# Kernel optimization log

Hardware: AMD Instinct MI355X
Metric: run time of the kernel (lower is better)

Reference implementation:

```python
import jax, jax.numpy as jnp
import numpy as np

# ---- static configuration (matches init_kwargs) ----
B = 256              # graph pairs -> 2B graphs total (query/corpus interleaved)
N_PER_GRAPH = 24     # nodes per graph
N_MAX = 32           # max node set size (transport plan side)
E_PER_GRAPH = 200    # edges per graph
E_MAX = 256          # max_edge_set_size
D_EDGE = 256         # edge_feature_dim
D_SINK = 256         # sinkhorn_feature_dim
TEMPERATURE = 0.1
NUM_SINKHORN_ITERS = 20
NOISE_FACTOR = 0.0   # deterministic sinkhorn
CONSISTENCY_WEIGHT = 1.0


def setup_inputs() -> dict:
    rng = np.random.RandomState(0)
    num_graphs = 2 * B
    node_offset = np.arange(num_graphs) * N_PER_GRAPH
    graph_idx = np.repeat(np.arange(num_graphs), N_PER_GRAPH)
    # edges are grouped by graph (standard batched-graph layout)
    from_local = rng.randint(0, N_PER_GRAPH, size=(num_graphs, E_PER_GRAPH))
    to_local = rng.randint(0, N_PER_GRAPH, size=(num_graphs, E_PER_GRAPH))
    from_idx = (from_local + node_offset[:, None]).reshape(-1)
    to_idx = (to_local + node_offset[:, None]).reshape(-1)
    total_edges = num_graphs * E_PER_GRAPH

    key = jax.random.key(0)
    k = jax.random.split(key, 4)
    return {
        "edge_features_enc": jax.random.normal(k[0], (total_edges, D_EDGE), jnp.float32),
        "node_transport_plan": jax.random.uniform(k[1], (B, N_MAX, N_MAX), jnp.float32),
        "W1": jax.random.normal(k[2], (D_EDGE, D_SINK), jnp.float32) / np.sqrt(D_EDGE).astype(np.float32),
        "b1": jnp.zeros((D_SINK,), jnp.float32),
        "W2": jax.random.normal(k[3], (D_SINK, D_SINK), jnp.float32) / np.sqrt(D_SINK).astype(np.float32),
        "b2": jnp.zeros((D_SINK,), jnp.float32),
        "from_idx": jnp.asarray(from_idx, jnp.int32),
        "to_idx": jnp.asarray(to_idx, jnp.int32),
        "graph_idx": jnp.asarray(graph_idx, jnp.int32),
        "query_sizes": jnp.full((B,), N_PER_GRAPH, jnp.int32),
        "corpus_sizes": jnp.full((B,), N_PER_GRAPH, jnp.int32),
    }


def reference(edge_features_enc, node_transport_plan, W1, b1, W2, b2,
              from_idx, to_idx, graph_idx, query_sizes, corpus_sizes):
    num_graphs = 2 * B
    total_edges = from_idx.shape[0]

    # --- get_paired_edge_counts / split_and_stack ---
    g_edge = graph_idx[from_idx]                                   # graph id per edge
    edge_counts = jax.ops.segment_sum(jnp.ones_like(g_edge), g_edge, num_segments=num_graphs)
    edge_offset = jnp.cumsum(edge_counts) - edge_counts            # exclusive prefix
    rank = jnp.arange(total_edges, dtype=jnp.int32) - edge_offset[g_edge]

    stacked = jnp.zeros((num_graphs, E_MAX, D_EDGE), edge_features_enc.dtype)
    stacked = stacked.at[g_edge, rank].set(edge_features_enc)      # [2B, E_MAX, D]
    q_feat, c_feat = stacked[0::2], stacked[1::2]

    # --- sinkhorn_feature_layers (Linear-ReLU-Linear) + size mask ---
    def mlp(x):
        return jax.nn.relu(x @ W1 + b1) @ W2 + b2
    q_feat, c_feat = mlp(q_feat), mlp(c_feat)
    pos = jnp.arange(E_MAX)
    q_feat = q_feat * (pos[None, :] < query_sizes[:, None]).astype(q_feat.dtype)[..., None]
    c_feat = c_feat * (pos[None, :] < corpus_sizes[:, None]).astype(c_feat.dtype)[..., None]

    # --- kronecker_product_on_nodes: local endpoint ids, pad slots -> zero row N_MAX ---
    node_counts = jax.ops.segment_sum(jnp.ones_like(graph_idx), graph_idx, num_segments=num_graphs)
    node_offset = jnp.cumsum(node_counts) - node_counts
    pad = jnp.full((num_graphs, E_MAX), N_MAX, jnp.int32)
    f_loc = pad.at[g_edge, rank].set(from_idx - node_offset[g_edge])
    t_loc = pad.at[g_edge, rank].set(to_idx - node_offset[g_edge])
    fq, fc = f_loc[0::2], f_loc[1::2]
    tq, tc = t_loc[0::2], t_loc[1::2]

    T = jnp.pad(node_transport_plan, ((0, 0), (0, 1), (0, 1)))     # zero row/col for pads
    b = jnp.arange(B)[:, None, None]
    straight = T[b, fq[:, :, None], fc[:, None, :]] * T[b, tq[:, :, None], tc[:, None, :]]
    cross = T[b, fq[:, :, None], tc[:, None, :]] * T[b, tq[:, :, None], fc[:, None, :]]

    # --- sinkhorn_iters (log domain, noise_factor=0) ---
    log_alpha = (straight + cross) / TEMPERATURE                   # [B, E_MAX, E_MAX]
    def step(la, _):
        la = la - jax.nn.logsumexp(la, axis=2, keepdims=True)
        la = la - jax.nn.logsumexp(la, axis=1, keepdims=True)
        return la, None
    log_alpha, _ = jax.lax.scan(step, log_alpha, None, length=NUM_SINKHORN_ITERS)
    plan = jnp.exp(log_alpha)

    # --- feature_alignment_score: -sum(relu(q - P c)) per pair ---
    score = -jax.nn.relu(q_feat - plan @ c_feat).sum(axis=(1, 2))
    return CONSISTENCY_WEIGHT * score
```

## Files before the change

### kernel.cpp

```cpp
#include <hip/hip_runtime.h>

typedef unsigned short ushort_t;
typedef unsigned int uint_t;

typedef float f32x4_t __attribute__((ext_vector_type(4)));
typedef short s16x8_t __attribute__((ext_vector_type(8)));

#define NB   256
#define NG   512
#define NPG  24
#define NMAXI 32
#define EPG  200
#define DD   256
#define L2E_OVER_T 14.426950408889634f

__device__ __forceinline__ ushort_t f2bf(float f) {
    uint_t u = __float_as_uint(f);
    u += 0x7FFFu + ((u >> 16) & 1u);
    return (ushort_t)(u >> 16);
}
__device__ __forceinline__ float bfhi(uint_t u) { return __uint_as_float(u & 0xFFFF0000u); }
__device__ __forceinline__ float bflo(uint_t u) { return __uint_as_float(u << 16); }

__device__ __forceinline__ float frcp(float x) {
#if __has_builtin(__builtin_amdgcn_rcpf)
    return __builtin_amdgcn_rcpf(x);
#else
    return 1.0f / x;
#endif
}

__global__ __launch_bounds__(256) void prep_w(const float* __restrict__ W1,
                                              const float* __restrict__ W2,
                                              ushort_t* __restrict__ W1T,
                                              ushort_t* __restrict__ W2T)
{
    __shared__ float tile[2][4 * 256];
    const int t = threadIdx.x;
    const int k0 = blockIdx.x * 4;
    #pragma unroll
    for (int i = t; i < 4 * 256; i += 256) {
        tile[0][i] = W1[k0 * 256 + i];
        tile[1][i] = W2[k0 * 256 + i];
    }
    __syncthreads();
    const int n = t;
    #pragma unroll
    for (int m = 0; m < 2; ++m) {
        uint_t p0 = (uint_t)f2bf(tile[m][0 * 256 + n]) | ((uint_t)f2bf(tile[m][1 * 256 + n]) << 16);
        uint_t p1 = (uint_t)f2bf(tile[m][2 * 256 + n]) | ((uint_t)f2bf(tile[m][3 * 256 + n]) << 16);
        ushort_t* dst = (m ? W2T : W1T) + n * 256 + k0;
        uint2 pk; pk.x = p0; pk.y = p1;
        *(uint2*)dst = pk;
    }
}

__global__ __launch_bounds__(256) void mlp_kernel(
    const float* __restrict__ X, const ushort_t* __restrict__ W1T,
    const ushort_t* __restrict__ W2T, const float* __restrict__ b1,
    const float* __restrict__ b2, float* __restrict__ Y)
{
    __shared__ ushort_t sA[64 * 272];
    const int t = threadIdx.x;
    const int blk = blockIdx.x;
    const int lane = t & 63;
    const int w = t >> 6;
    const int quad = lane >> 4;
    const int mrow = lane & 15;

    {
        int r = t >> 2;
        int ch = (t & 3) * 64;
        int rho = blk * 64 + r;
        int g = rho / NPG;
        int e = rho - g * NPG;
        const float* src = X + ((size_t)(g * EPG + e)) * DD + ch;
        ushort_t* dst = &sA[r * 272 + ch];
        #pragma unroll
        for (int i = 0; i < 8; ++i) {
            float4 v0 = *(const float4*)(src + i * 8);
            float4 v1 = *(const float4*)(src + i * 8 + 4);
            uint4 pk;
            pk.x = (uint_t)f2bf(v0.x) | ((uint_t)f2bf(v0.y) << 16);
            pk.y = (uint_t)f2bf(v0.z) | ((uint_t)f2bf(v0.w) << 16);
            pk.z = (uint_t)f2bf(v1.x) | ((uint_t)f2bf(v1.y) << 16);
            pk.w = (uint_t)f2bf(v1.z) | ((uint_t)f2bf(v1.w) << 16);
            *(uint4*)(dst + i * 8) = pk;
        }
    }
    __syncthreads();

    f32x4_t acc[16];
    #pragma unroll
    for (int i = 0; i < 16; ++i) acc[i] = (f32x4_t){0.f, 0.f, 0.f, 0.f};

    #pragma unroll
    for (int k0 = 0; k0 < 256; k0 += 32) {
        s16x8_t a[4], bb[4];
        #pragma unroll
        for (int mt = 0; mt < 4; ++mt)
            a[mt] = *(const s16x8_t*)&sA[(mt * 16 + mrow) * 272 + k0 + quad * 8];
        #pragma unroll
        for (int nt = 0; nt < 4; ++nt)
            bb[nt] = *(const s16x8_t*)(W1T + (size_t)(64 * w + nt * 16 + mrow) * 256 + k0 + quad * 8);
        #pragma unroll
        for (int mt = 0; mt < 4; ++mt) {
            #pragma unroll
            for (int nt = 0; nt < 4; ++nt)
                acc[mt * 4 + nt] = __builtin_amdgcn_mfma_f32_16x16x32_bf16(
                    a[mt], bb[nt], acc[mt * 4 + nt], 0, 0, 0);
        }
    }
    __syncthreads();

    #pragma unroll
    for (int nt = 0; nt < 4; ++nt) {
        int col = 64 * w + nt * 16 + mrow;
        float bias = b1[col];
        #pragma unroll
        for (int mt = 0; mt < 4; ++mt) {
            f32x4_t v = acc[mt * 4 + nt];
            #pragma unroll
            for (int reg = 0; reg < 4; ++reg) {
                int row = mt * 16 + quad * 4 + reg;
                sA[row * 272 + col] = f2bf(fmaxf(v[reg] + bias, 0.f));
            }
        }
    }
    __syncthreads();

    #pragma unroll
    for (int i = 0; i < 16; ++i) acc[i] = (f32x4_t){0.f, 0.f, 0.f, 0.f};

    #pragma unroll
    for (int k0 = 0; k0 < 256; k0 += 32) {
        s16x8_t a[4], bb[4];
        #pragma unroll
        for (int mt = 0; mt < 4; ++mt)
            a[mt] = *(const s16x8_t*)&sA[(mt * 16 + mrow) * 272 + k0 + quad * 8];
        #pragma unroll
        for (int nt = 0; nt < 4; ++nt)
            bb[nt] = *(const s16x8_t*)(W2T + (size_t)(64 * w + nt * 16 + mrow) * 256 + k0 + quad * 8);
        #pragma unroll
        for (int mt = 0; mt < 4; ++mt) {
            #pragma unroll
            for (int nt = 0; nt < 4; ++nt)
                acc[mt * 4 + nt] = __builtin_amdgcn_mfma_f32_16x16x32_bf16(
                    a[mt], bb[nt], acc[mt * 4 + nt], 0, 0, 0);
        }
    }

    #pragma unroll
    for (int nt = 0; nt < 4; ++nt) {
        int col = 64 * w + nt * 16 + mrow;
        float bias = b2[col];
        #pragma unroll
        for (int mt = 0; mt < 4; ++mt) {
            f32x4_t v = acc[mt * 4 + nt];
            #pragma unroll
            for (int reg = 0; reg < 4; ++reg) {
                int row = blk * 64 + mt * 16 + quad * 4 + reg;
                Y[(size_t)row * 256 + col] = v[reg] + bias;
            }
        }
    }
}

__global__ __launch_bounds__(1024) void sink_kernel(
    const float* __restrict__ Tplan, const int* __restrict__ from_idx,
    const int* __restrict__ to_idx, const int* __restrict__ qsz,
    const int* __restrict__ csz, const float* __restrict__ qcf,
    float* __restrict__ out)
{
    const int b = blockIdx.x;
    const int t = threadIdx.x;
    const int R = t >> 4;
    const int C = t & 15;
    const int w = t >> 6;

    __shared__ __align__(16) char ovl[56320];
    __shared__ float ru_s[260];
    __shared__ float rv_p[320];
    __shared__ float wsum[16];

    float* Tl = (float*)ovl;
    int* fq = (int*)(ovl + 4368);
    int* tq = (int*)(ovl + 5392);
    int* fc = (int*)(ovl + 6416);
    int* tc = (int*)(ovl + 7440);
    float* Vp = (float*)ovl;
    ushort_t* planb = (ushort_t*)ovl;
    ushort_t* cftb  = (ushort_t*)(ovl + 20480);

    for (int i = t; i < 33 * 33; i += 1024) Tl[i] = 0.f;
    if (t < 320) rv_p[t] = 1.0f;
    if (t < 256) {
        int gq = 2 * b, gc = 2 * b + 1;
        int a = NMAXI, bb = NMAXI, c = NMAXI, d = NMAXI;
        if (t < EPG) {
            a  = from_idx[gq * EPG + t] - gq * NPG;
            bb = to_idx  [gq * EPG + t] - gq * NPG;
            c  = from_idx[gc * EPG + t] - gc * NPG;
            d  = to_idx  [gc * EPG + t] - gc * NPG;
        }
        fq[t] = a; tq[t] = bb; fc[t] = c; tc[t] = d;
    }
    __syncthreads();
    {
        int i = t >> 5, j = t & 31;
        Tl[i * 33 + j] = Tplan[((size_t)b << 10) + t];
    }
    __syncthreads();

    uint_t Kp[4][8];
    {
        const float* T1a = &Tl[fq[4 * R + 0] * 33];
        const float* T2a = &Tl[tq[4 * R + 0] * 33];
        const float* T1b = &Tl[fq[4 * R + 1] * 33];
        const float* T2b = &Tl[tq[4 * R + 1] * 33];
        const float* T1c = &Tl[fq[4 * R + 2] * 33];
        const float* T2c = &Tl[tq[4 * R + 2] * 33];
        const float* T1d = &Tl[fq[4 * R + 3] * 33];
        const float* T2d = &Tl[tq[4 * R + 3] * 33];
        #pragma unroll
        for (int u = 0; u < 8; ++u) {
            int c0 = 16 * C + 2 * u;
            int f0 = fc[c0], t0 = tc[c0];
            int f1 = fc[c0 + 1], t1 = tc[c0 + 1];
            float la;
            la = T1a[f0] * T2a[t0] + T1a[t0] * T2a[f0];
            float e00 = exp2f(la * L2E_OVER_T);
            la = T1a[f1] * T2a[t1] + T1a[t1] * T2a[f1];
            Kp[0][u] = (uint_t)f2bf(e00) | ((uint_t)f2bf(exp2f(la * L2E_OVER_T)) << 16);
            la = T1b[f0] * T2b[t0] + T1b[t0] * T2b[f0];
            float e10 = exp2f(la * L2E_OVER_T);
            la = T1b[f1] * T2b[t1] + T1b[t1] * T2b[f1];
            Kp[1][u] = (uint_t)f2bf(e10) | ((uint_t)f2bf(exp2f(la * L2E_OVER_T)) << 16);
            la = T1c[f0] * T2c[t0] + T1c[t0] * T2c[f0];
            float e20 = exp2f(la * L2E_OVER_T);
            la = T1c[f1] * T2c[t1] + T1c[t1] * T2c[f1];
            Kp[2][u] = (uint_t)f2bf(e20) | ((uint_t)f2bf(exp2f(la * L2E_OVER_T)) << 16);
            la = T1d[f0] * T2d[t0] + T1d[t0] * T2d[f0];
            float e30 = exp2f(la * L2E_OVER_T);
            la = T1d[f1] * T2d[t1] + T1d[t1] * T2d[f1];
            Kp[3][u] = (uint_t)f2bf(e30) | ((uint_t)f2bf(exp2f(la * L2E_OVER_T)) << 16);
        }
    }

    for (int it = 0; it < 20; ++it) {
        {
            float4 rv0 = *(const float4*)&rv_p[20 * C + 0];
            float4 rv1 = *(const float4*)&rv_p[20 * C + 4];
            float4 rv2 = *(const float4*)&rv_p[20 * C + 8];
            float4 rv3 = *(const float4*)&rv_p[20 * C + 12];
            float pr[4];
            #pragma unroll
            for (int i = 0; i < 4; ++i) {
                float a0 = bflo(Kp[i][0]) * rv0.x + bfhi(Kp[i][0]) * rv0.y;
                float a1 = bflo(Kp[i][1]) * rv0.z + bfhi(Kp[i][1]) * rv0.w;
                float a2 = bflo(Kp[i][2]) * rv1.x + bfhi(Kp[i][2]) * rv1.y;
                float a3 = bflo(Kp[i][3]) * rv1.z + bfhi(Kp[i][3]) * rv1.w;
                a0 += bflo(Kp[i][4]) * rv2.x + bfhi(Kp[i][4]) * rv2.y;
                a1 += bflo(Kp[i][5]) * rv2.z + bfhi(Kp[i][5]) * rv2.w;
                a2 += bflo(Kp[i][6]) * rv3.x + bfhi(Kp[i][6]) * rv3.y;
                a3 += bflo(Kp[i][7]) * rv3.z + bfhi(Kp[i][7]) * rv3.w;
                pr[i] = (a0 + a1) + (a2 + a3);
            }
            #pragma unroll
            for (int i = 0; i < 4; ++i) {
                float s = pr[i];
                s += __shfl_xor(s, 1);
                s += __shfl_xor(s, 2);
                s += __shfl_xor(s, 4);
                s += __shfl_xor(s, 8);
                pr[i] = s;
            }
            if (C == 0) {
                #pragma unroll
                for (int i = 0; i < 4; ++i) ru_s[4 * R + i] = frcp(pr[i]);
            }
        }
        __syncthreads();
        {
            float u0 = ru_s[4 * R + 0], u1 = ru_s[4 * R + 1];
            float u2 = ru_s[4 * R + 2], u3 = ru_s[4 * R + 3];
            float pc[16];
            #pragma unroll
            for (int u = 0; u < 8; ++u) {
                float e0 = bflo(Kp[0][u]) * u0 + bflo(Kp[1][u]) * u1
                         + bflo(Kp[2][u]) * u2 + bflo(Kp[3][u]) * u3;
                float e1 = bfhi(Kp[0][u]) * u0 + bfhi(Kp[1][u]) * u1
                         + bfhi(Kp[2][u]) * u2 + bfhi(Kp[3][u]) * u3;
                pc[2 * u] = e0; pc[2 * u + 1] = e1;
            }
            #pragma unroll
            for (int k = 0; k < 16; ++k) {
                float s = pc[k];
                s += __shfl_xor(s, 16);
                s += __shfl_xor(s, 32);
                pc[k] = s;
            }
            if ((t & 63) < 16) {
                float* dst = &Vp[w * 272 + C * 16];
                *(float4*)(dst + 0)  = (float4){pc[0], pc[1], pc[2], pc[3]};
                *(float4*)(dst + 4)  = (float4){pc[4], pc[5], pc[6], pc[7]};
                *(float4*)(dst + 8)  = (float4){pc[8], pc[9], pc[10], pc[11]};
                *(float4*)(dst + 12) = (float4){pc[12], pc[13], pc[14], pc[15]};
            }
        }
        __syncthreads();
        if (t < 256) {
            float s = 0.f;
            #pragma unroll
            for (int ww = 0; ww < 16; ++ww) s += Vp[ww * 272 + t];
            rv_p[(t >> 4) * 20 + (t & 15)] = frcp(s);
        }
        __syncthreads();
    }

    int nq = qsz[b]; if (nq > 24) nq = 24;
    int nc = csz[b]; if (nc > 24) nc = 24;

    {
        uint_t* z = (uint_t*)ovl;
        #pragma unroll
        for (int k = 0; k < 10; ++k) z[t + 1024 * k] = 0u;
    }
    __syncthreads();

    if (C < 2) {
        int umax = (C == 0) ? 8 : 4;
        #pragma unroll
        for (int i = 0; i < 4; ++i) {
            int row = 4 * R + i;
            float rr = ru_s[row];
            for (int u = 0; u < umax; ++u) {
                int j = 16 * C + 2 * u;
                float p0 = (j < nc)     ? bflo(Kp[i][u]) * rr * rv_p[20 * C + 2 * u]     : 0.f;
                float p1 = (j + 1 < nc) ? bfhi(Kp[i][u]) * rr * rv_p[20 * C + 2 * u + 1] : 0.f;
                *(uint_t*)(planb + row * 40 + j) =
                    (uint_t)f2bf(p0) | ((uint_t)f2bf(p1) << 16);
            }
        }
    }
    if (t < 768) {
        int j = t >> 5, inner = t & 31;
        int c0 = inner * 8;
        const float* src = qcf + ((size_t)(2 * b + 1) * 24 + j) * 256 + c0;
        float4 v0 = *(const float4*)(src);
        float4 v1 = *(const float4*)(src + 4);
        cftb[(c0 + 0) * 40 + j] = f2bf(v0.x);
        cftb[(c0 + 1) * 40 + j] = f2bf(v0.y);
        cftb[(c0 + 2) * 40 + j] = f2bf(v0.z);
        cftb[(c0 + 3) * 40 + j] = f2bf(v0.w);
        cftb[(c0 + 4) * 40 + j] = f2bf(v1.x);
        cftb[(c0 + 5) * 40 + j] = f2bf(v1.y);
        cftb[(c0 + 6) * 40 + j] = f2bf(v1.z);
        cftb[(c0 + 7) * 40 + j] = f2bf(v1.w);
    }
    __syncthreads();

    const int lane = t & 63;
    const int mrow = lane & 15;
    const int quad = lane >> 4;
    float ssum = 0.f;
    {
        const float* qbase = qcf + (size_t)(2 * b) * 24 * 256;
        s16x8_t a = *(const s16x8_t*)(planb + (16 * w + mrow) * 40 + quad * 8);
        #pragma unroll
        for (int nt = 0; nt < 16; ++nt) {
            s16x8_t bbf = *(const s16x8_t*)(cftb + (16 * nt + mrow) * 40 + quad * 8);
            f32x4_t acc = (f32x4_t){0.f, 0.f, 0.f, 0.f};
            acc = __builtin_amdgcn_mfma_f32_16x16x32_bf16(a, bbf, acc, 0, 0, 0);
            int col = 16 * nt + mrow;
            #pragma unroll
            for (int reg = 0; reg < 4; ++reg) {
                int row = 16 * w + quad * 4 + reg;
                if (row < nq) {
                    float qv = qbase[(size_t)row * 256 + col];
                    ssum += fmaxf(qv - acc[reg], 0.f);
                } else {
                    ssum += fmaxf(-acc[reg], 0.f);
                }
            }
        }
    }
    ssum += __shfl_xor(ssum, 1);
    ssum += __shfl_xor(ssum, 2);
    ssum += __shfl_xor(ssum, 4);
    ssum += __shfl_xor(ssum, 8);
    ssum += __shfl_xor(ssum, 16);
    ssum += __shfl_xor(ssum, 32);
    if (lane == 0) wsum[w] = ssum;
    __syncthreads();
    if (t == 0) {
        float s = 0.f;
        #pragma unroll
        for (int i = 0; i < 16; ++i) s += wsum[i];
        out[b] = -s;
    }
}

extern "C" void kernel_launch(void* const* d_in, const int* in_sizes, int n_in,
                              void* d_out, int out_size, void* d_ws, size_t ws_size,
                              hipStream_t stream)
{
    const float* edge_feat = (const float*)d_in[0];
    const float* tplan     = (const float*)d_in[1];
    const float* W1        = (const float*)d_in[2];
    const float* b1        = (const float*)d_in[3];
    const float* W2        = (const float*)d_in[4];
    const float* b2        = (const float*)d_in[5];
    const int*   from_idx  = (const int*)d_in[6];
    const int*   to_idx    = (const int*)d_in[7];
    const int*   qsz       = (const int*)d_in[9];
    const int*   csz       = (const int*)d_in[10];
    float* out = (float*)d_out;

    char* ws = (char*)d_ws;
    ushort_t* W1T = (ushort_t*)ws;
    ushort_t* W2T = W1T + 65536;
    float* qcf = (float*)(ws + 262144);

    prep_w<<<64, 256, 0, stream>>>(W1, W2, W1T, W2T);
    mlp_kernel<<<192, 256, 0, stream>>>(edge_feat, W1T, W2T, b1, b2, qcf);
    sink_kernel<<<256, 1024, 0, stream>>>(tplan, from_idx, to_idx, qsz, csz, qcf, out);
}
```

Measured before the change: 280.4 us.

## Halve sinkhorn block to 512 threads with 8 rows of kernel per thread

The sinkhorn kernel now runs 512 threads per block instead of 1024. Each thread holds 8 rows of the bf16 kernel matrix in registers instead of 4, and each wave computes two MFMA row tiles in the final score. Loops that stage data and zero memory are adjusted for the smaller block. The aim is to cut cross-wave reduction and barrier cost and to raise per-thread work in the 20 Sinkhorn iterations, at the cost of doubled register pressure (64 packed values per thread) and fewer waves to hide latency.

```diff
diff --git a/kernel.cpp b/kernel.cpp
--- a/kernel.cpp
+++ b/kernel.cpp
@@ -166,7 +166,7 @@
     }
 }
 
-__global__ __launch_bounds__(1024) void sink_kernel(
+__global__ __launch_bounds__(512) void sink_kernel(
     const float* __restrict__ Tplan, const int* __restrict__ from_idx,
     const int* __restrict__ to_idx, const int* __restrict__ qsz,
     const int* __restrict__ csz, const float* __restrict__ qcf,
@@ -181,7 +181,7 @@
     __shared__ __align__(16) char ovl[56320];
     __shared__ float ru_s[260];
     __shared__ float rv_p[320];
-    __shared__ float wsum[16];
+    __shared__ float wsum[8];
 
     float* Tl = (float*)ovl;
     int* fq = (int*)(ovl + 4368);
@@ -192,7 +192,7 @@
     ushort_t* planb = (ushort_t*)ovl;
     ushort_t* cftb  = (ushort_t*)(ovl + 20480);
 
-    for (int i = t; i < 33 * 33; i += 1024) Tl[i] = 0.f;
+    for (int i = t; i < 33 * 33; i += 512) Tl[i] = 0.f;
     if (t < 320) rv_p[t] = 1.0f;
     if (t < 256) {
         int gq = 2 * b, gc = 2 * b + 1;
@@ -207,43 +207,29 @@
     }
     __syncthreads();
     {
-        int i = t >> 5, j = t & 31;
-        Tl[i * 33 + j] = Tplan[((size_t)b << 10) + t];
-    }
-    __syncthreads();
-
-    uint_t Kp[4][8];
-    {
-        const float* T1a = &Tl[fq[4 * R + 0] * 33];
-        const float* T2a = &Tl[tq[4 * R + 0] * 33];
-        const float* T1b = &Tl[fq[4 * R + 1] * 33];
-        const float* T2b = &Tl[tq[4 * R + 1] * 33];
-        const float* T1c = &Tl[fq[4 * R + 2] * 33];
-        const float* T2c = &Tl[tq[4 * R + 2] * 33];
-        const float* T1d = &Tl[fq[4 * R + 3] * 33];
-        const float* T2d = &Tl[tq[4 * R + 3] * 33];
+        #pragma unroll
+        for (int h = 0; h < 2; ++h) {
+            int idx = t + 512 * h;
+            int i = idx >> 5, j = idx & 31;
+            Tl[i * 33 + j] = Tplan[((size_t)b << 10) + idx];
+        }
+    }
+    __syncthreads();
+
+    uint_t Kp[8][8];
+    #pragma unroll
+    for (int i = 0; i < 8; ++i) {
+        const float* T1 = &Tl[fq[8 * R + i] * 33];
+        const float* T2 = &Tl[tq[8 * R + i] * 33];
         #pragma unroll
         for (int u = 0; u < 8; ++u) {
             int c0 = 16 * C + 2 * u;
             int f0 = fc[c0], t0 = tc[c0];
             int f1 = fc[c0 + 1], t1 = tc[c0 + 1];
-            float la;
-            la = T1a[f0] * T2a[t0] + T1a[t0] * T2a[f0];
-            float e00 = exp2f(la * L2E_OVER_T);
-            la = T1a[f1] * T2a[t1] + T1a[t1] * T2a[f1];
-            Kp[0][u] = (uint_t)f2bf(e00) | ((uint_t)f2bf(exp2f(la * L2E_OVER_T)) << 16);
-            la = T1b[f0] * T2b[t0] + T1b[t0] * T2b[f0];
-            float e10 = exp2f(la * L2E_OVER_T);
-            la = T1b[f1] * T2b[t1] + T1b[t1] * T2b[f1];
-            Kp[1][u] = (uint_t)f2bf(e10) | ((uint_t)f2bf(exp2f(la * L2E_OVER_T)) << 16);
-            la = T1c[f0] * T2c[t0] + T1c[t0] * T2c[f0];
-            float e20 = exp2f(la * L2E_OVER_T);
-            la = T1c[f1] * T2c[t1] + T1c[t1] * T2c[f1];
-            Kp[2][u] = (uint_t)f2bf(e20) | ((uint_t)f2bf(exp2f(la * L2E_OVER_T)) << 16);
-            la = T1d[f0] * T2d[t0] + T1d[t0] * T2d[f0];
-            float e30 = exp2f(la * L2E_OVER_T);
-            la = T1d[f1] * T2d[t1] + T1d[t1] * T2d[f1];
-            Kp[3][u] = (uint_t)f2bf(e30) | ((uint_t)f2bf(exp2f(la * L2E_OVER_T)) << 16);
+            float la0 = T1[f0] * T2[t0] + T1[t0] * T2[f0];
+            float la1 = T1[f1] * T2[t1] + T1[t1] * T2[f1];
+            Kp[i][u] = (uint_t)f2bf(exp2f(la0 * L2E_OVER_T))
+                     | ((uint_t)f2bf(exp2f(la1 * L2E_OVER_T)) << 16);
         }
     }
 
@@ -253,9 +239,8 @@
             float4 rv1 = *(const float4*)&rv_p[20 * C + 4];
             float4 rv2 = *(const float4*)&rv_p[20 * C + 8];
             float4 rv3 = *(const float4*)&rv_p[20 * C + 12];
-            float pr[4];
-            #pragma unroll
-            for (int i = 0; i < 4; ++i) {
+            #pragma unroll
+            for (int i = 0; i < 8; ++i) {
                 float a0 = bflo(Kp[i][0]) * rv0.x + bfhi(Kp[i][0]) * rv0.y;
                 float a1 = bflo(Kp[i][1]) * rv0.z + bfhi(Kp[i][1]) * rv0.w;
                 float a2 = bflo(Kp[i][2]) * rv1.x + bfhi(Kp[i][2]) * rv1.y;
@@ -264,34 +249,27 @@
                 a1 += bflo(Kp[i][5]) * rv2.z + bfhi(Kp[i][5]) * rv2.w;
                 a2 += bflo(Kp[i][6]) * rv3.x + bfhi(Kp[i][6]) * rv3.y;
                 a3 += bflo(Kp[i][7]) * rv3.z + bfhi(Kp[i][7]) * rv3.w;
-                pr[i] = (a0 + a1) + (a2 + a3);
-            }
-            #pragma unroll
-            for (int i = 0; i < 4; ++i) {
-                float s = pr[i];
+                float s = (a0 + a1) + (a2 + a3);
                 s += __shfl_xor(s, 1);
                 s += __shfl_xor(s, 2);
                 s += __shfl_xor(s, 4);
                 s += __shfl_xor(s, 8);
-                pr[i] = s;
-            }
-            if (C == 0) {
-                #pragma unroll
-                for (int i = 0; i < 4; ++i) ru_s[4 * R + i] = frcp(pr[i]);
+                if (C == 0) ru_s[8 * R + i] = frcp(s);
             }
         }
         __syncthreads();
         {
-            float u0 = ru_s[4 * R + 0], u1 = ru_s[4 * R + 1];
-            float u2 = ru_s[4 * R + 2], u3 = ru_s[4 * R + 3];
             float pc[16];
             #pragma unroll
-            for (int u = 0; u < 8; ++u) {
-                float e0 = bflo(Kp[0][u]) * u0 + bflo(Kp[1][u]) * u1
-                         + bflo(Kp[2][u]) * u2 + bflo(Kp[3][u]) * u3;
-                float e1 = bfhi(Kp[0][u]) * u0 + bfhi(Kp[1][u]) * u1
-                         + bfhi(Kp[2][u]) * u2 + bfhi(Kp[3][u]) * u3;
-                pc[2 * u] = e0; pc[2 * u + 1] = e1;
+            for (int u = 0; u < 8; ++u) { pc[2 * u] = 0.f; pc[2 * u + 1] = 0.f; }
+            #pragma unroll
+            for (int i = 0; i < 8; ++i) {
+                float ui = ru_s[8 * R + i];
+                #pragma unroll
+                for (int u = 0; u < 8; ++u) {
+                    pc[2 * u]     += bflo(Kp[i][u]) * ui;
+                    pc[2 * u + 1] += bfhi(Kp[i][u]) * ui;
+                }
             }
             #pragma unroll
             for (int k = 0; k < 16; ++k) {
@@ -312,7 +290,7 @@
         if (t < 256) {
             float s = 0.f;
             #pragma unroll
-            for (int ww = 0; ww < 16; ++ww) s += Vp[ww * 272 + t];
+            for (int ww = 0; ww < 8; ++ww) s += Vp[ww * 272 + t];
             rv_p[(t >> 4) * 20 + (t & 15)] = frcp(s);
         }
         __syncthreads();
@@ -324,15 +302,15 @@
     {
         uint_t* z = (uint_t*)ovl;
         #pragma unroll
-        for (int k = 0; k < 10; ++k) z[t + 1024 * k] = 0u;
+        for (int k = 0; k < 20; ++k) z[t + 512 * k] = 0u;
     }
     __syncthreads();
 
     if (C < 2) {
         int umax = (C == 0) ? 8 : 4;
         #pragma unroll
-        for (int i = 0; i < 4; ++i) {
-            int row = 4 * R + i;
+        for (int i = 0; i < 8; ++i) {
+            int row = 8 * R + i;
             float rr = ru_s[row];
             for (int u = 0; u < umax; ++u) {
                 int j = 16 * C + 2 * u;
@@ -343,20 +321,24 @@
             }
         }
     }
-    if (t < 768) {
-        int j = t >> 5, inner = t & 31;
-        int c0 = inner * 8;
-        const float* src = qcf + ((size_t)(2 * b + 1) * 24 + j) * 256 + c0;
-        float4 v0 = *(const float4*)(src);
-        float4 v1 = *(const float4*)(src + 4);
-        cftb[(c0 + 0) * 40 + j] = f2bf(v0.x);
-        cftb[(c0 + 1) * 40 + j] = f2bf(v0.y);
-        cftb[(c0 + 2) * 40 + j] = f2bf(v0.z);
-        cftb[(c0 + 3) * 40 + j] = f2bf(v0.w);
-        cftb[(c0 + 4) * 40 + j] = f2bf(v1.x);
-        cftb[(c0 + 5) * 40 + j] = f2bf(v1.y);
-        cftb[(c0 + 6) * 40 + j] = f2bf(v1.z);
-        cftb[(c0 + 7) * 40 + j] = f2bf(v1.w);
+    #pragma unroll
+    for (int h = 0; h < 2; ++h) {
+        int idx = t + 512 * h;
+        if (idx < 768) {
+            int j = idx >> 5, inner = idx & 31;
+            int c0 = inner * 8;
+            const float* src = qcf + ((size_t)(2 * b + 1) * 24 + j) * 256 + c0;
+            float4 v0 = *(const float4*)(src);
+            float4 v1 = *(const float4*)(src + 4);
+            cftb[(c0 + 0) * 40 + j] = f2bf(v0.x);
+            cftb[(c0 + 1) * 40 + j] = f2bf(v0.y);
+            cftb[(c0 + 2) * 40 + j] = f2bf(v0.z);
+            cftb[(c0 + 3) * 40 + j] = f2bf(v0.w);
+            cftb[(c0 + 4) * 40 + j] = f2bf(v1.x);
+            cftb[(c0 + 5) * 40 + j] = f2bf(v1.y);
+            cftb[(c0 + 6) * 40 + j] = f2bf(v1.z);
+            cftb[(c0 + 7) * 40 + j] = f2bf(v1.w);
+        }
     }
     __syncthreads();
 
@@ -366,16 +348,29 @@
     float ssum = 0.f;
     {
         const float* qbase = qcf + (size_t)(2 * b) * 24 * 256;
-        s16x8_t a = *(const s16x8_t*)(planb + (16 * w + mrow) * 40 + quad * 8);
+        s16x8_t a0 = *(const s16x8_t*)(planb + (32 * w + mrow) * 40 + quad * 8);
+        s16x8_t a1 = *(const s16x8_t*)(planb + (32 * w + 16 + mrow) * 40 + quad * 8);
         #pragma unroll
         for (int nt = 0; nt < 16; ++nt) {
             s16x8_t bbf = *(const s16x8_t*)(cftb + (16 * nt + mrow) * 40 + quad * 8);
+            int col = 16 * nt + mrow;
             f32x4_t acc = (f32x4_t){0.f, 0.f, 0.f, 0.f};
-            acc = __builtin_amdgcn_mfma_f32_16x16x32_bf16(a, bbf, acc, 0, 0, 0);
-            int col = 16 * nt + mrow;
+            acc = __builtin_amdgcn_mfma_f32_16x16x32_bf16(a0, bbf, acc, 0, 0, 0);
             #pragma unroll
             for (int reg = 0; reg < 4; ++reg) {
-                int row = 16 * w + quad * 4 + reg;
+                int row = 32 * w + quad * 4 + reg;
+                if (row < nq) {
+                    float qv = qbase[(size_t)row * 256 + col];
+                    ssum += fmaxf(qv - acc[reg], 0.f);
+                } else {
+                    ssum += fmaxf(-acc[reg], 0.f);
+                }
+            }
+            acc = (f32x4_t){0.f, 0.f, 0.f, 0.f};
+            acc = __builtin_amdgcn_mfma_f32_16x16x32_bf16(a1, bbf, acc, 0, 0, 0);
+            #pragma unroll
+            for (int reg = 0; reg < 4; ++reg) {
+                int row = 32 * w + 16 + quad * 4 + reg;
                 if (row < nq) {
                     float qv = qbase[(size_t)row * 256 + col];
                     ssum += fmaxf(qv - acc[reg], 0.f);
@@ -396,7 +391,7 @@
     if (t == 0) {
         float s = 0.f;
         #pragma unroll
-        for (int i = 0; i < 16; ++i) s += wsum[i];
+        for (int i = 0; i < 8; ++i) s += wsum[i];
         out[b] = -s;
     }
 }
@@ -424,5 +419,5 @@
 
     prep_w<<<64, 256, 0, stream>>>(W1, W2, W1T, W2T);
     mlp_kernel<<<192, 256, 0, stream>>>(edge_feat, W1T, W2T, b1, b2, qcf);
-    sink_kernel<<<256, 1024, 0, stream>>>(tplan, from_idx, to_idx, qsz, csz, qcf, out);
-}
+    sink_kernel<<<256, 512, 0, stream>>>(tplan, from_idx, to_idx, qsz, csz, qcf, out);
+}
```

Result: slower. 308.2 us (+9.9%).
